# Kernel tuning notes

Hardware: AMD Instinct MI355X
Metric: run time of the kernel (lower is better)

## Reference

```python
import jax, jax.numpy as jnp
import numpy as np

B, S, H = 2, 4096, 2048
NH, NKV, D = 16, 4, 128
BS, LOCAL, GLOB, STRIDE = 64, 8, 4, 16
SEL = GLOB + LOCAL
SCALE = D ** -0.5
NEG = -1e9


def rotate_half(x):
    x1, x2 = x[..., : D // 2], x[..., D // 2 :]
    return jnp.concatenate([-x2, x1], axis=-1)


def setup_inputs():
    key = jax.random.key(0)
    ks = jax.random.split(key, 5)
    hidden_states = jax.random.normal(ks[0], (B, S, H), dtype=jnp.float32)
    # standard RoPE tables, shape [B, S, D] as the module expects (cos.unsqueeze(1))
    pos = jnp.arange(S, dtype=jnp.float32)
    inv = 1.0 / (10000.0 ** (jnp.arange(0, D, 2, dtype=jnp.float32) / D))
    freqs = pos[:, None] * inv[None, :]
    emb = jnp.concatenate([freqs, freqs], axis=-1)
    cos = jnp.broadcast_to(jnp.cos(emb)[None], (B, S, D)).astype(jnp.float32)
    sin = jnp.broadcast_to(jnp.sin(emb)[None], (B, S, D)).astype(jnp.float32)
    std = 0.02
    Wq = jax.random.normal(ks[1], (NH * D, H), dtype=jnp.float32) * std
    Wk = jax.random.normal(ks[2], (NKV * D, H), dtype=jnp.float32) * std
    Wv = jax.random.normal(ks[3], (NKV * D, H), dtype=jnp.float32) * std
    Wo = jax.random.normal(ks[4], (H, NH * D), dtype=jnp.float32) * std
    return {"hidden_states": hidden_states, "cos": cos, "sin": sin,
            "Wq": Wq, "Wk": Wk, "Wv": Wv, "Wo": Wo}


def _block_sparse_attn(q, k, v):
    # q, k, v: [B, NH, S, D]; past_len = 0, attention_mask = None (all keys valid)
    qb = S // BS
    kb = S // BS
    qid = jnp.arange(qb)
    # local blocks: the LOCAL most recent blocks ending at the query block
    loc = qid[:, None] - (LOCAL - 1 - jnp.arange(LOCAL)[None, :])
    loc = jnp.clip(loc, 0, kb - 1)
    # global blocks: strided anchors
    g = jnp.clip(jnp.arange(GLOB) * STRIDE, 0, kb - 1)
    glob = jnp.broadcast_to(g[None, :], (qb, GLOB))
    sel = jnp.concatenate([glob, loc], axis=1)  # [qb, SEL]
    valid = sel <= qid[:, None]                 # causal at block level
    # dedup: drop a selected block if an earlier slot selected the same block
    eq = sel[:, :, None] == sel[:, None, :]
    lower = jnp.tril(jnp.ones((SEL, SEL), dtype=bool), k=-1)
    keep = (~(eq & lower[None]).any(-1)) & valid  # [qb, SEL]

    k_blk = k.reshape(B, NH, kb, BS, D)
    v_blk = v.reshape(B, NH, kb, BS, D)
    k_sel = jnp.take(k_blk, sel.reshape(-1), axis=2).reshape(B, NH, qb, SEL * BS, D)
    v_sel = jnp.take(v_blk, sel.reshape(-1), axis=2).reshape(B, NH, qb, SEL * BS, D)
    q_blk = q.reshape(B, NH, qb, BS, D)

    scores = jnp.einsum("bhqid,bhqjd->bhqij", q_blk, k_sel) * SCALE  # [B,NH,qb,BS,SEL*BS]
    keep_tok = jnp.broadcast_to(keep[:, :, None], (qb, SEL, BS)).reshape(qb, SEL * BS)
    scores = scores + (1.0 - keep_tok.astype(scores.dtype))[None, None, :, None, :] * NEG
    # intra-block causal mask where selected block == query block
    same = (sel == qid[:, None]).astype(scores.dtype)  # [qb, SEL]
    intra = jnp.triu(jnp.full((BS, BS), NEG, dtype=scores.dtype), k=1)
    scores6 = scores.reshape(B, NH, qb, BS, SEL, BS)
    scores6 = scores6 + intra[None, None, None, :, None, :] * same[None, None, :, None, :, None]
    scores = scores6.reshape(B, NH, qb, BS, SEL * BS)
    probs = jax.nn.softmax(scores, axis=-1)
    out = jnp.einsum("bhqij,bhqjd->bhqid", probs, v_sel)
    return out.reshape(B, NH, S, D)


def reference(hidden_states, cos, sin, Wq, Wk, Wv, Wo):
    q = (hidden_states @ Wq.T).reshape(B, S, NH, D).transpose(0, 2, 1, 3)
    k = (hidden_states @ Wk.T).reshape(B, S, NKV, D).transpose(0, 2, 1, 3)
    v = (hidden_states @ Wv.T).reshape(B, S, NKV, D).transpose(0, 2, 1, 3)
    c = cos[:, None, :, :]
    s = sin[:, None, :, :]
    q = q * c + rotate_half(q) * s
    k = k * c + rotate_half(k) * s
    rep = NH // NKV
    k = jnp.repeat(k, rep, axis=1)
    v = jnp.repeat(v, rep, axis=1)
    out = _block_sparse_attn(q, k, v)
    out = out.transpose(0, 2, 1, 3).reshape(B, S, NH * D)
    return out @ Wo.T
```

## Files before the change

kernel.cpp:

```cpp
#include <hip/hip_runtime.h>

typedef __bf16 bf16_t;
typedef __bf16 bf16x8_t __attribute__((ext_vector_type(8)));
typedef __bf16 bf16x4_t __attribute__((ext_vector_type(4)));
typedef float f32x4_t __attribute__((ext_vector_type(4)));
typedef unsigned short u16;
typedef unsigned int u32;

#define B_ 2
#define S_ 4096
#define NH_ 16
#define NKV_ 4
#define D_ 128
#define NEG_ (-1000000000.0f)
#define SCALE_ 0.08838834764831845f

__device__ __forceinline__ void load16(const bf16_t* g, bf16_t* l) {
  __builtin_amdgcn_global_load_lds(
      (__attribute__((address_space(1))) void*)(g),
      (__attribute__((address_space(3))) void*)(l),
      16, 0, 0);
}

__global__ __launch_bounds__(256) void cvt_all_kernel(const float* __restrict__ hs,
                                                      const float* __restrict__ Wq,
                                                      const float* __restrict__ Wk,
                                                      const float* __restrict__ Wv,
                                                      const float* __restrict__ Wo,
                                                      bf16_t* __restrict__ Xb,
                                                      bf16_t* __restrict__ Wb,
                                                      bf16_t* __restrict__ Wob) {
  int i = blockIdx.x * 256 + threadIdx.x;
  const float* src; bf16_t* dst; int local;
  if (i < 4194304)      { src = hs; dst = Xb;            local = i; }
  else if (i < 5242880) { src = Wq; dst = Wb;            local = i - 4194304; }
  else if (i < 5505024) { src = Wk; dst = Wb + 4194304;  local = i - 5242880; }
  else if (i < 5767168) { src = Wv; dst = Wb + 5242880;  local = i - 5505024; }
  else                  { src = Wo; dst = Wob;           local = i - 5767168; }
  float4 v = ((const float4*)src)[local];
  bf16x4_t o;
  o.x = (bf16_t)v.x; o.y = (bf16_t)v.y; o.z = (bf16_t)v.z; o.w = (bf16_t)v.w;
  *(bf16x4_t*)(dst + (size_t)local * 4) = o;
}


#define SB0() __builtin_amdgcn_sched_barrier(0)
#define BAR_MID() { SB0(); __builtin_amdgcn_s_barrier(); \
  asm volatile("s_waitcnt lgkmcnt(0)" ::: "memory"); SB0(); }
#define BAR_END() { SB0(); __builtin_amdgcn_s_barrier(); SB0(); }
#define BAR_END_VM() { SB0(); asm volatile("s_waitcnt vmcnt(4)" ::: "memory"); \
  __builtin_amdgcn_s_barrier(); SB0(); }

#define LDA_(BUF, MP) { \
  _Pragma("unroll") for (int mi = 0; mi < 4; mi++) { \
    _Pragma("unroll") for (int ks = 0; ks < 2; ks++) { \
      a[mi][ks] = *(const bf16x8_t*)&As[BUF][ks][wr * 128 + (MP) * 64 + mi * 16 + l15][(l4 ^ xr) * 8]; } } }

#define LDB_(BUF, NP) { \
  _Pragma("unroll") for (int n2 = 0; n2 < 2; n2++) { \
    _Pragma("unroll") for (int ks = 0; ks < 2; ks++) { \
      b[(NP) * 2 + n2][ks] = *(const bf16x8_t*)&Bs[BUF][ks][wc * 64 + (NP) * 32 + n2 * 16 + l15][(l4 ^ xr) * 8]; } } }

#define MFMA_Q(MP, NP) { \
  __builtin_amdgcn_s_setprio(1); \
  _Pragma("unroll") for (int mi = 0; mi < 4; mi++) { \
    _Pragma("unroll") for (int n2 = 0; n2 < 2; n2++) { \
      _Pragma("unroll") for (int ks = 0; ks < 2; ks++) { \
        acc[(MP) * 4 + mi][(NP) * 2 + n2] = __builtin_amdgcn_mfma_f32_16x16x32_bf16( \
            a[mi][ks], b[(NP) * 2 + n2][ks], acc[(MP) * 4 + mi][(NP) * 2 + n2], 0, 0, 0); } } } \
  __builtin_amdgcn_s_setprio(0); }

template <int BF16OUT>
__global__ __launch_bounds__(512, 2) void gemm256_kernel(const bf16_t* __restrict__ A,
                                                         const bf16_t* __restrict__ Bm,
                                                         float* __restrict__ Cf,
                                                         bf16_t* __restrict__ Cb,
                                                         int M, int N, int K) {
  __shared__ __align__(16) bf16_t As[2][2][256][32];
  __shared__ __align__(16) bf16_t Bs[2][2][256][32];
  const int t = threadIdx.x;
  const int lane = t & 63;
  const int w = t >> 6;
  const int wr = w >> 2;
  const int wc = w & 3;
  const int l15 = lane & 15, l4 = lane >> 4;
  const int xr = (l15 >> 1) & 3;
  const int sp = w >> 2;
  const int swi = w & 3;
  const int srow = lane >> 2;
  const int sg = lane & 3;
  const int scg = (srow >> 1) & 3;

  const int m0 = blockIdx.x * 256;
  const int n0 = blockIdx.y * 256;

  const bf16_t* Ablk = A + (size_t)m0 * K;
  const bf16_t* Bblk = Bm + (size_t)n0 * K;

  f32x4_t acc[8][4] = {};
  bf16x8_t a[4][2], b[4][2];

  const int nkt = K >> 6;
  const int nit = nkt >> 1;

  auto stageA = [&](int buf, int mp, int kt) {
#pragma unroll
    for (int c = 0; c < 2; c++) {
      int r0 = c * 128 + mp * 64;
      load16(Ablk + (size_t)(r0 + swi * 16 + srow) * K + kt * 64 + sp * 32 + (sg ^ scg) * 8,
             &As[buf][0][0][0] + sp * 8192 + (r0 + swi * 16) * 32);
    }
  };
  auto stageB = [&](int buf, int np, int kt) {
#pragma unroll
    for (int c = 0; c < 2; c++) {
      int r0 = (c * 2 + (swi >> 1)) * 64 + np * 32 + (swi & 1) * 16;
      load16(Bblk + (size_t)(r0 + srow) * K + kt * 64 + sp * 32 + (sg ^ scg) * 8,
             &Bs[buf][0][0][0] + sp * 8192 + r0 * 32);
    }
  };

  stageA(0, 0, 0); stageB(0, 0, 0); stageA(0, 1, 0); stageB(0, 1, 0);
  stageA(1, 0, 1); stageB(1, 0, 1);
  asm volatile("s_waitcnt vmcnt(4)" ::: "memory");
  __builtin_amdgcn_s_barrier();
  SB0();

#pragma unroll 1
  for (int i = 0; i < nit; i++) {
    const int ktA = 2 * i + 1;
    const int ktB = (2 * i + 2 < nkt) ? 2 * i + 2 : nkt - 1;
    const int ktC = (2 * i + 3 < nkt) ? 2 * i + 3 : nkt - 1;
    LDA_(0, 0); LDB_(0, 0); stageA(1, 1, ktA);
    BAR_MID(); MFMA_Q(0, 0); BAR_END();
    LDB_(0, 1); stageB(1, 1, ktA);
    BAR_MID(); MFMA_Q(0, 1); BAR_END();
    LDA_(0, 1); stageA(0, 0, ktB);
    BAR_MID(); MFMA_Q(1, 0); BAR_END();
    stageB(0, 0, ktB);
    BAR_MID(); MFMA_Q(1, 1); BAR_END_VM();
    LDA_(1, 0); LDB_(1, 0); stageA(0, 1, ktB);
    BAR_MID(); MFMA_Q(0, 0); BAR_END();
    LDB_(1, 1); stageB(0, 1, ktB);
    BAR_MID(); MFMA_Q(0, 1); BAR_END();
    LDA_(1, 1); stageA(1, 0, ktC);
    BAR_MID(); MFMA_Q(1, 0); BAR_END();
    stageB(1, 0, ktC);
    BAR_MID(); MFMA_Q(1, 1); BAR_END_VM();
  }

#pragma unroll
  for (int ar = 0; ar < 8; ar++)
#pragma unroll
    for (int ni = 0; ni < 4; ni++)
#pragma unroll
      for (int r = 0; r < 4; r++) {
        int grow = m0 + wr * 128 + (ar >> 2) * 64 + (ar & 3) * 16 + l4 * 4 + r;
        int gcol = n0 + wc * 64 + ni * 16 + l15;
        float v = acc[ar][ni][r];
        if (BF16OUT) Cb[(size_t)grow * N + gcol] = (bf16_t)v;
        else Cf[(size_t)grow * N + gcol] = v;
      }
}

__global__ __launch_bounds__(320) void rope_kernel(const bf16_t* __restrict__ qkv,
                                                   const float* __restrict__ cosp,
                                                   const float* __restrict__ sinp,
                                                   bf16_t* __restrict__ Qro,
                                                   bf16_t* __restrict__ Kro) {
  const int tk = blockIdx.x;
  const int b = tk >> 12;
  const int s = tk & 4095;
  const int sblock = s >> 6, row = s & 63;
  const int idx = threadIdx.x;
  int head, lc;
  const bf16_t* base;
  bf16_t* outp;
  if (idx < 256) {
    head = idx >> 4; lc = idx & 15;
    base = qkv + (size_t)tk * 3072 + head * 128;
    outp = Qro + ((size_t)(b * NH_ + head) * 64 + sblock) * 8192;
  } else {
    int i2 = idx - 256;
    head = i2 >> 4; lc = i2 & 15;
    base = qkv + (size_t)tk * 3072 + 2048 + head * 128;
    outp = Kro + ((size_t)(b * NKV_ + head) * 64 + sblock) * 8192;
  }
  const int d0 = lc * 8;
  bf16x8_t x = *(const bf16x8_t*)(base + d0);
  const int d0p = (d0 < 64) ? d0 + 64 : d0 - 64;
  bf16x8_t xp = *(const bf16x8_t*)(base + d0p);
  const float sgn = (d0 < 64) ? -1.0f : 1.0f;
  const float* cb = cosp + (size_t)tk * 128 + d0;
  const float* sb = sinp + (size_t)tk * 128 + d0;
  bf16x8_t o;
#pragma unroll
  for (int e = 0; e < 8; e++)
    o[e] = (bf16_t)((float)x[e] * cb[e] + sgn * (float)xp[e] * sb[e]);
  *(bf16x8_t*)(outp + (lc * 64 + row) * 8) = o;
}

__global__ __launch_bounds__(256) void vtrans_kernel(const u16* __restrict__ qkv,
                                                     u16* __restrict__ vt) {
  __shared__ u16 tile[64][136];
  const int sblock = blockIdx.x;
  const int kh = blockIdx.y;
  const int b = blockIdx.z;
  const int t = threadIdx.x;
#pragma unroll
  for (int i = 0; i < 4; i++) {
    int f = t + 256 * i;
    int sl = f >> 4, c = f & 15;
    uint4 vv = *(const uint4*)(qkv + (size_t)(b * S_ + sblock * 64 + sl) * 3072 + 2560 + kh * 128 + c * 8);
    *(uint4*)&tile[sl][c * 8] = vv;
  }
  __syncthreads();
  u16* out = vt + ((size_t)(b * NKV_ + kh) * 64 + sblock) * 8192;
#pragma unroll
  for (int i = 0; i < 4; i++) {
    int g = t + 256 * i;
    int sc = g >> 7, d = g & 127;
    u16 e0 = tile[sc * 8 + 0][d], e1 = tile[sc * 8 + 1][d];
    u16 e2 = tile[sc * 8 + 2][d], e3 = tile[sc * 8 + 3][d];
    u16 e4 = tile[sc * 8 + 4][d], e5 = tile[sc * 8 + 5][d];
    u16 e6 = tile[sc * 8 + 6][d], e7 = tile[sc * 8 + 7][d];
    uint4 ov;
    ov.x = (u32)e0 | ((u32)e1 << 16);
    ov.y = (u32)e2 | ((u32)e3 << 16);
    ov.z = (u32)e4 | ((u32)e5 << 16);
    ov.w = (u32)e6 | ((u32)e7 << 16);
    *(uint4*)(out + (size_t)g * 8) = ov;
  }
}

__global__ __launch_bounds__(256) void attn_kernel(const bf16_t* __restrict__ Qr,
                                                   const bf16_t* __restrict__ Kr,
                                                   const bf16_t* __restrict__ Vt,
                                                   bf16_t* __restrict__ Ao) {
  __shared__ bf16_t Ks[2][8192];
  __shared__ bf16_t Vs[2][8192];
  __shared__ bf16_t Ps[4 * 16 * 72];
  const int qid = blockIdx.x;
  const int kh = blockIdx.y >> 1;
  const int hp = blockIdx.y & 1;
  const int b = blockIdx.z;
  const int t = threadIdx.x;
  const int lane = t & 63;
  const int w = t >> 6;
  const int l15 = lane & 15, l4 = lane >> 4;
  const int h = kh * 4 + hp * 2 + (w >> 1);
  int row0[2];
  row0[0] = ((w * 2) & 3) * 16;
  row0[1] = ((w * 2 + 1) & 3) * 16;

  int list[12];
  int nkeep = 0;
#pragma unroll
  for (int j = 0; j < 12; j++) {
    int cj;
    if (j < 4) cj = j * 16;
    else { cj = qid - 11 + j; cj = cj < 0 ? 0 : cj; cj = cj > 63 ? 63 : cj; }
    bool keep = (cj <= qid);
#pragma unroll
    for (int i = 0; i < j; i++) {
      int ci;
      if (i < 4) ci = i * 16;
      else { ci = qid - 11 + i; ci = ci < 0 ? 0 : ci; ci = ci > 63 ? 63 : ci; }
      if (ci == cj) keep = false;
    }
    if (keep) list[nkeep++] = cj;
  }

  const bf16_t* Qg = Qr + ((size_t)(b * NH_ + h) * 64 + qid) * 8192;
  const bf16_t* Kg = Kr + ((size_t)(b * NKV_ + kh) * 64) * 8192;
  const bf16_t* Vg = Vt + ((size_t)(b * NKV_ + kh) * 64) * 8192;

  bf16x8_t qa[2][4];
#pragma unroll
  for (int mt = 0; mt < 2; mt++)
#pragma unroll
    for (int ks = 0; ks < 4; ks++)
      qa[mt][ks] = *(const bf16x8_t*)(Qg + ((ks * 4 + l4) * 64 + row0[mt] + l15) * 8);

  bf16x8_t ones;
#pragma unroll
  for (int e = 0; e < 8; e++) ones[e] = (bf16_t)1.0f;

  float mi_r[2][4], li_r[2][4];
  f32x4_t oacc[2][8] = {};
#pragma unroll
  for (int mt = 0; mt < 2; mt++)
#pragma unroll
    for (int r = 0; r < 4; r++) { mi_r[mt][r] = -__builtin_inff(); li_r[mt][r] = 0.0f; }

  {
    int cj = list[0];
#pragma unroll
    for (int i = 0; i < 4; i++) {
      int f = t + 256 * i;
      load16(Kg + (size_t)cj * 8192 + (size_t)f * 8, Ks[0] + (w * 64 + i * 256) * 8);
      load16(Vg + (size_t)cj * 8192 + (size_t)f * 8, Vs[0] + (w * 64 + i * 256) * 8);
    }
  }

  int cur = 0;
#pragma unroll 1
  for (int idx = 0; idx < nkeep; idx++) {
    const int cj = list[idx];
    __syncthreads();
    if (idx + 1 < nkeep) {
      int cn = list[idx + 1];
#pragma unroll
      for (int i = 0; i < 4; i++) {
        int f = t + 256 * i;
        load16(Kg + (size_t)cn * 8192 + (size_t)f * 8, Ks[cur ^ 1] + (w * 64 + i * 256) * 8);
        load16(Vg + (size_t)cn * 8192 + (size_t)f * 8, Vs[cur ^ 1] + (w * 64 + i * 256) * 8);
      }
    }
    const bf16_t* ks_ = Ks[cur];
    const bf16_t* vs_ = Vs[cur];

    f32x4_t sacc[2][4] = {};
#pragma unroll
    for (int ks = 0; ks < 4; ks++)
#pragma unroll
      for (int ni = 0; ni < 4; ni++) {
        bf16x8_t kb = *(const bf16x8_t*)&ks_[((ks * 4 + l4) * 64 + ni * 16 + l15) * 8];
#pragma unroll
        for (int mt = 0; mt < 2; mt++)
          sacc[mt][ni] = __builtin_amdgcn_mfma_f32_16x16x32_bf16(qa[mt][ks], kb, sacc[mt][ni], 0, 0, 0);
      }

    const bool diag = (cj == qid);
    float alpha[2][4];
#pragma unroll
    for (int mt = 0; mt < 2; mt++) {
      float sv[4][4];
#pragma unroll
      for (int ni = 0; ni < 4; ni++)
#pragma unroll
        for (int r = 0; r < 4; r++) {
          float x = sacc[mt][ni][r] * SCALE_;
          if (diag && (ni * 16 + l15) > (row0[mt] + l4 * 4 + r)) x += NEG_;
          sv[ni][r] = x;
        }

      float rmax[4];
#pragma unroll
      for (int r = 0; r < 4; r++)
        rmax[r] = fmaxf(fmaxf(sv[0][r], sv[1][r]), fmaxf(sv[2][r], sv[3][r]));
#pragma unroll
      for (int msk = 1; msk < 16; msk <<= 1)
#pragma unroll
        for (int r = 0; r < 4; r++)
          rmax[r] = fmaxf(rmax[r], __shfl_xor(rmax[r], msk, 64));
#pragma unroll
      for (int r = 0; r < 4; r++) {
        float nm = fmaxf(mi_r[mt][r], rmax[r]);
        alpha[mt][r] = __expf(mi_r[mt][r] - nm);
        mi_r[mt][r] = nm;
      }
      float p[4][4];
#pragma unroll
      for (int ni = 0; ni < 4; ni++)
#pragma unroll
        for (int r = 0; r < 4; r++)
          p[ni][r] = __expf(sv[ni][r] - mi_r[mt][r]);
#pragma unroll
      for (int ni = 0; ni < 4; ni++)
#pragma unroll
        for (int r = 0; r < 4; r++)
          Ps[w * 1152 + (l4 * 4 + r) * 72 + ni * 16 + l15] = (bf16_t)p[ni][r];
#pragma unroll
      for (int n2 = 0; n2 < 8; n2++)
#pragma unroll
        for (int r = 0; r < 4; r++)
          oacc[mt][n2][r] *= alpha[mt][r];

      f32x4_t lacc = {};
#pragma unroll
      for (int kst = 0; kst < 2; kst++) {
        bf16x8_t pa = *(const bf16x8_t*)&Ps[w * 1152 + l15 * 72 + kst * 32 + l4 * 8];
        lacc = __builtin_amdgcn_mfma_f32_16x16x32_bf16(pa, ones, lacc, 0, 0, 0);
#pragma unroll
        for (int n2 = 0; n2 < 8; n2++) {
          bf16x8_t vb = *(const bf16x8_t*)&vs_[((kst * 4 + l4) * 128 + n2 * 16 + l15) * 8];
          oacc[mt][n2] = __builtin_amdgcn_mfma_f32_16x16x32_bf16(pa, vb, oacc[mt][n2], 0, 0, 0);
        }
      }
#pragma unroll
      for (int r = 0; r < 4; r++)
        li_r[mt][r] = li_r[mt][r] * alpha[mt][r] + lacc[r];
    }

    cur ^= 1;
  }

#pragma unroll
  for (int mt = 0; mt < 2; mt++) {
    float invl[4];
#pragma unroll
    for (int r = 0; r < 4; r++) invl[r] = 1.0f / li_r[mt][r];
#pragma unroll
    for (int n2 = 0; n2 < 8; n2++)
#pragma unroll
      for (int r = 0; r < 4; r++) {
        int m = row0[mt] + l4 * 4 + r;
        size_t idx = ((size_t)(b * S_ + qid * 64 + m)) * (NH_ * D_) + h * D_ + n2 * 16 + l15;
        Ao[idx] = (bf16_t)(oacc[mt][n2][r] * invl[r]);
      }
  }
}

extern "C" void kernel_launch(void* const* d_in, const int* in_sizes, int n_in,
                              void* d_out, int out_size, void* d_ws, size_t ws_size,
                              hipStream_t stream) {
  const float* hs = (const float*)d_in[0];
  const float* cosp = (const float*)d_in[1];
  const float* sinp = (const float*)d_in[2];
  const float* Wq = (const float*)d_in[3];
  const float* Wk = (const float*)d_in[4];
  const float* Wv = (const float*)d_in[5];
  const float* Wo = (const float*)d_in[6];
  float* outp = (float*)d_out;

  char* ws = (char*)d_ws;
  bf16_t* Xb   = (bf16_t*)(ws);
  bf16_t* Wb   = (bf16_t*)(ws + 33554432);
  bf16_t* Wob  = (bf16_t*)(ws + 46137344);
  bf16_t* QKVo = (bf16_t*)(ws + 54525952);
  bf16_t* Qr   = (bf16_t*)(ws + 104857600);
  bf16_t* Kr   = (bf16_t*)(ws + 138412032);
  bf16_t* Vt   = (bf16_t*)(ws + 146800640);
  bf16_t* Ao   = QKVo;

  cvt_all_kernel<<<dim3(26624), dim3(256), 0, stream>>>(hs, Wq, Wk, Wv, Wo, Xb, Wb, Wob);

  gemm256_kernel<1><<<dim3(32, 12), dim3(512), 0, stream>>>(Xb, Wb, (float*)nullptr, QKVo,
                                                            8192, 3072, 2048);
  rope_kernel<<<dim3(8192), dim3(320), 0, stream>>>(QKVo, cosp, sinp, Qr, Kr);
  vtrans_kernel<<<dim3(64, NKV_, B_), dim3(256), 0, stream>>>((const u16*)QKVo, (u16*)Vt);
  attn_kernel<<<dim3(64, NKV_ * 2, B_), dim3(256), 0, stream>>>(Qr, Kr, Vt, Ao);
  gemm256_kernel<0><<<dim3(32, 8), dim3(512), 0, stream>>>(Ao, Wob, outp, (bf16_t*)nullptr,
                                                           8192, 2048, 2048);
}
```

Before: 526.8 us.

## Restructure GEMM main loop with fewer barriers and merged MFMA phases

Rewrites the double-buffered bf16 GEMM loop so that each K-half runs two MFMA quadrants per phase. This cuts per-iteration workgroup barriers from sixteen to four. It also removes the explicit sched_barriers and lgkmcnt waits, letting the compiler interleave LDS reads, global-to-LDS staging and MFMAs on its own. The vmcnt drains move to the start of each buffer switch, and a final vmcnt(0) is added before the epilogue. The risk is that the compiler interleaves less well without the sched_barriers, that more A/B fragments stay live in registers at once, and that the buffer-hazard ordering becomes harder to keep correct.

```diff
diff --git a/kernel.cpp b/kernel.cpp
--- a/kernel.cpp
+++ b/kernel.cpp
@@ -44,12 +44,8 @@
 }
 
 
-#define SB0() __builtin_amdgcn_sched_barrier(0)
-#define BAR_MID() { SB0(); __builtin_amdgcn_s_barrier(); \
-  asm volatile("s_waitcnt lgkmcnt(0)" ::: "memory"); SB0(); }
-#define BAR_END() { SB0(); __builtin_amdgcn_s_barrier(); SB0(); }
-#define BAR_END_VM() { SB0(); asm volatile("s_waitcnt vmcnt(4)" ::: "memory"); \
-  __builtin_amdgcn_s_barrier(); SB0(); }
+#define DRAIN4() asm volatile("s_waitcnt vmcnt(4)" ::: "memory")
+#define BARF() { __builtin_amdgcn_s_barrier(); asm volatile("" ::: "memory"); }
 
 #define LDA_(BUF, MP) { \
   _Pragma("unroll") for (int mi = 0; mi < 4; mi++) { \
@@ -122,32 +118,30 @@
 
   stageA(0, 0, 0); stageB(0, 0, 0); stageA(0, 1, 0); stageB(0, 1, 0);
   stageA(1, 0, 1); stageB(1, 0, 1);
-  asm volatile("s_waitcnt vmcnt(4)" ::: "memory");
-  __builtin_amdgcn_s_barrier();
-  SB0();
 
 #pragma unroll 1
   for (int i = 0; i < nit; i++) {
     const int ktA = 2 * i + 1;
     const int ktB = (2 * i + 2 < nkt) ? 2 * i + 2 : nkt - 1;
     const int ktC = (2 * i + 3 < nkt) ? 2 * i + 3 : nkt - 1;
-    LDA_(0, 0); LDB_(0, 0); stageA(1, 1, ktA);
-    BAR_MID(); MFMA_Q(0, 0); BAR_END();
-    LDB_(0, 1); stageB(1, 1, ktA);
-    BAR_MID(); MFMA_Q(0, 1); BAR_END();
-    LDA_(0, 1); stageA(0, 0, ktB);
-    BAR_MID(); MFMA_Q(1, 0); BAR_END();
-    stageB(0, 0, ktB);
-    BAR_MID(); MFMA_Q(1, 1); BAR_END_VM();
-    LDA_(1, 0); LDB_(1, 0); stageA(0, 1, ktB);
-    BAR_MID(); MFMA_Q(0, 0); BAR_END();
-    LDB_(1, 1); stageB(0, 1, ktB);
-    BAR_MID(); MFMA_Q(0, 1); BAR_END();
-    LDA_(1, 1); stageA(1, 0, ktC);
-    BAR_MID(); MFMA_Q(1, 0); BAR_END();
-    stageB(1, 0, ktC);
-    BAR_MID(); MFMA_Q(1, 1); BAR_END_VM();
-  }
+    DRAIN4(); BARF();
+    LDA_(0, 0); LDB_(0, 0); LDB_(0, 1);
+    stageA(1, 1, ktA); stageB(1, 1, ktA);
+    MFMA_Q(0, 0); MFMA_Q(0, 1);
+    BARF();
+    LDA_(0, 1);
+    stageB(0, 1, ktB); stageB(0, 0, ktB);
+    MFMA_Q(1, 0); MFMA_Q(1, 1);
+    DRAIN4(); BARF();
+    LDA_(1, 0); LDB_(1, 0); LDB_(1, 1);
+    stageA(0, 1, ktB); stageA(0, 0, ktB);
+    MFMA_Q(0, 0); MFMA_Q(0, 1);
+    BARF();
+    LDA_(1, 1);
+    stageA(1, 0, ktC); stageB(1, 0, ktC);
+    MFMA_Q(1, 0); MFMA_Q(1, 1);
+  }
+  asm volatile("s_waitcnt vmcnt(0)" ::: "memory");
 
 #pragma unroll
   for (int ar = 0; ar < 8; ar++)
```

Result: faster. 504.8 us (-4.2%).
